# Optimization experiments

Hardware: AMD Instinct MI355X
Metric: run time of the kernel (lower is better)

Reference implementation:

```python
import jax, jax.numpy as jnp
import numpy as np

IN_C = 128
OUT_C = 128
N = 100000
E = 1600000


def spmm(row, col, w, x, n):
    # out[i] = sum_{e: row[e]==i} w[e] * x[col[e]]  (sparse adjacency matmul)
    return jax.ops.segment_sum(w[:, None] * x[col], row, num_segments=n)


def setup_inputs() -> dict:
    key = jax.random.key(0)
    ks = jax.random.split(key, 10)
    x = jax.random.normal(ks[0], (N, IN_C), dtype=jnp.float32)
    row = jax.random.randint(ks[1], (E,), 0, N, dtype=jnp.int32)
    col = jax.random.randint(ks[2], (E,), 0, N, dtype=jnp.int32)
    edge_weight = jax.random.uniform(ks[3], (E,), dtype=jnp.float32)
    s = 1.0 / np.sqrt(IN_C)
    W0 = jax.random.uniform(ks[4], (IN_C, OUT_C), minval=-s, maxval=s, dtype=jnp.float32)
    b0 = jax.random.uniform(ks[5], (OUT_C,), minval=-s, maxval=s, dtype=jnp.float32)
    W1 = jax.random.uniform(ks[6], (IN_C, OUT_C), minval=-s, maxval=s, dtype=jnp.float32)
    b1 = jax.random.uniform(ks[7], (OUT_C,), minval=-s, maxval=s, dtype=jnp.float32)
    W2 = jax.random.uniform(ks[8], (IN_C, OUT_C), minval=-s, maxval=s, dtype=jnp.float32)
    b2 = jax.random.uniform(ks[9], (OUT_C,), minval=-s, maxval=s, dtype=jnp.float32)
    return {"x": x, "row": row, "col": col, "edge_weight": edge_weight,
            "W0": W0, "b0": b0, "W1": W1, "b1": b1, "W2": W2, "b2": b2}


def reference(x, row, col, edge_weight, W0, b0, W1, b1, W2, b2):
    n = x.shape[0]
    # hop 0: plain linear
    x0 = x @ W0 + b0
    # hop 1: linear then one SpMM propagation
    x1 = spmm(row, col, edge_weight, x @ W1 + b1, n)
    # hop 2: linear then two SpMM propagations
    x2 = spmm(row, col, edge_weight,
              spmm(row, col, edge_weight, x @ W2 + b2, n), n)
    return jnp.concatenate([x0, x1, x2], axis=1)  # [N, 3*OUT_C]
```

## Files before the change

kernel.cpp:

```cpp
#include <hip/hip_runtime.h>

typedef __attribute__((ext_vector_type(8))) short bf16x8;
typedef __attribute__((ext_vector_type(4))) float f32x4;
typedef __attribute__((ext_vector_type(2))) float f32x2;
typedef __attribute__((ext_vector_type(2))) uint u32x2;

static inline size_t align256(size_t x) { return (x + 255) & ~size_t(255); }

__device__ inline ushort f2bf(float f) {
  uint u = __float_as_uint(f);
  return (ushort)((u + 0x7FFFu + ((u >> 16) & 1u)) >> 16);
}
__device__ inline float bf2f(ushort h) { return __uint_as_float(((uint)h) << 16); }


__device__ inline uint fp8x4_enc(float a0, float a1, float a2, float a3) {
#if __has_builtin(__builtin_amdgcn_cvt_pk_fp8_f32)
  int v = 0;
  v = __builtin_amdgcn_cvt_pk_fp8_f32(a0, a1, v, false);
  v = __builtin_amdgcn_cvt_pk_fp8_f32(a2, a3, v, true);
  return (uint)v;
#else
  float a[4] = {a0, a1, a2, a3};
  uint r = 0;
#pragma unroll
  for (int k = 0; k < 4; ++k) {
    uint u = __float_as_uint(a[k]);
    uint s = (u >> 24) & 0x80u;
    uint au = u & 0x7FFFFFFFu;
    uint b;
    if (au < 0x3C800000u) {
      b = s;
    } else {
      uint rr = au + 0x7FFFFu + ((au >> 20) & 1u);
      uint e = (rr >> 23) - 120u;
      uint m = (rr >> 20) & 7u;
      b = s | (e << 3) | m;
    }
    r |= b << (8 * k);
  }
  return r;
#endif
}

__device__ inline f32x4 fp8x4_dec(uint u) {
  f32x4 r;
#if __has_builtin(__builtin_amdgcn_cvt_pk_f32_fp8)
  auto lo = __builtin_amdgcn_cvt_pk_f32_fp8((int)u, false);
  auto hi = __builtin_amdgcn_cvt_pk_f32_fp8((int)u, true);
  r[0] = lo[0]; r[1] = lo[1]; r[2] = hi[0]; r[3] = hi[1];
#else
#pragma unroll
  for (int k = 0; k < 4; ++k) {
    uint b = (u >> (8 * k)) & 0xFFu;
    uint f = ((b & 0x80u) << 24) | (((b & 0x7Fu) + (120u << 3)) << 20);
    r[k] = (b & 0x7Fu) ? __uint_as_float(f) : 0.f;
  }
#endif
  return r;
}

__device__ inline float ew_dec(uint u) { return __uint_as_float((u & 0x7FFFu) << 16); }

#define BW_SHIFT 7
#define NBUCK_MAX 1024
#define NCHUNK 256
#define PREP_BLOCKS 96


__global__ __launch_bounds__(512) void build_a_kernel(
    const int* __restrict__ row, int* __restrict__ bcnt,
    int* __restrict__ chunk_hist, int E, int chunk,
    const float* __restrict__ W0, const float* __restrict__ W1,
    const float* __restrict__ W2, ushort* __restrict__ Wt,
    int* __restrict__ done, int* __restrict__ boff, int* __restrict__ gcur,
    int* __restrict__ offp, int n) {
  __shared__ int h[NBUCK_MAX];
  int bid = blockIdx.x;
  int t = threadIdx.x;
  if (bid < NCHUNK) {
    for (int i = t; i < NBUCK_MAX; i += 512) h[i] = 0;
    __syncthreads();
    int c0 = bid * chunk, c1 = min(c0 + chunk, E);
    for (int i = c0 + t; i < c1; i += 512)
      atomicAdd(&h[row[i] >> BW_SHIFT], 1);
    __syncthreads();
    for (int i = t; i < NBUCK_MAX; i += 512) {
      int c = h[i];
      chunk_hist[bid * NBUCK_MAX + i] = c;
      if (c) atomicAdd(&bcnt[i], c);
    }
  } else {
    int i = (bid - NCHUNK) * 512 + t;
    int mat = i >> 14, r = i & 16383;
    int k = r >> 7, c = r & 127;
    const float* W = (mat == 0) ? W0 : (mat == 1) ? W1 : W2;
    Wt[mat * 16384 + c * 128 + k] = f2bf(W[k * 128 + c]);
  }
  __shared__ int ticket;
  __syncthreads();
  if (t == 0) {
    __threadfence();
    ticket = atomicAdd(done, 1);
  }
  __syncthreads();
  if (ticket == (int)gridDim.x - 1) {
    __threadfence();
    int v0 = bcnt[2 * t], v1 = bcnt[2 * t + 1];
    int pair = v0 + v1;
    h[t] = pair;
    __syncthreads();
    for (int o = 1; o < 512; o <<= 1) {
      int a = (t >= o) ? h[t - o] : 0;
      __syncthreads();
      h[t] += a;
      __syncthreads();
    }
    int excl = h[t] - pair;
    boff[2 * t] = excl;          gcur[2 * t] = excl;
    boff[2 * t + 1] = excl + v0; gcur[2 * t + 1] = excl + v0;
    if (t == 511) boff[NBUCK_MAX] = E;
    if (t == 0) offp[n] = E;
  }
}


__global__ __launch_bounds__(512) void bin_scatter(
    const int* __restrict__ row, const int* __restrict__ col,
    const float* __restrict__ w, int* __restrict__ gcur,
    const int* __restrict__ chunk_hist, int2* __restrict__ es_tmp,
    int E, int chunk) {
  __shared__ int lbase[NBUCK_MAX];
  __shared__ int lh[NBUCK_MAX];
  int bid = blockIdx.x;
  int t = threadIdx.x;
  for (int i = t; i < NBUCK_MAX; i += 512) {
    int c = chunk_hist[bid * NBUCK_MAX + i];
    lbase[i] = c ? atomicAdd(&gcur[i], c) : 0;
    lh[i] = 0;
  }
  __syncthreads();
  int c0 = bid * chunk, c1 = min(c0 + chunk, E);
  for (int i = c0 + t; i < c1; i += 512) {
    int r = row[i];
    int b = r >> BW_SHIFT;
    int pos = lbase[b] + atomicAdd(&lh[b], 1);
    es_tmp[pos] = make_int2(((r & 127) << 17) | col[i], __float_as_int(w[i]));
  }
}


__global__ __launch_bounds__(256) void sort_gemm_kernel(
    const int2* __restrict__ es_tmp, const int* __restrict__ boff,
    uint* __restrict__ es, int* __restrict__ offp, int ng,
    const float* __restrict__ x, const ushort* __restrict__ Wt,
    const float* __restrict__ b0, const float* __restrict__ b1,
    const float* __restrict__ b2,
    float* __restrict__ out0, unsigned char* __restrict__ y12, int n) {
  int t = threadIdx.x;
  if ((int)blockIdx.x >= ng) {
    __shared__ int lh[128];
    __shared__ int lex[128];
    int b = (int)blockIdx.x - ng;
    int base = boff[b], cnt = boff[b + 1] - base;
    if (t < 128) lh[t] = 0;
    __syncthreads();
    for (int i = t; i < cnt; i += 256)
      atomicAdd(&lh[(es_tmp[base + i].x >> 17) & 127], 1);
    __syncthreads();
    if (t < 128) lex[t] = lh[t];
    __syncthreads();
    for (int o = 1; o < 128; o <<= 1) {
      int a = (t >= o && t < 128) ? lex[t - o] : 0;
      __syncthreads();
      if (t < 128) lex[t] += a;
      __syncthreads();
    }
    if (t < 128) {
      int v = lh[t];
      int excl = lex[t] - v;
      int node = (b << BW_SHIFT) + t;
      if (node < n) offp[node] = base + excl;
      lh[t] = excl;
    }
    __syncthreads();
    for (int i = t; i < cnt; i += 256) {
      int2 ed = es_tmp[base + i];
      int nl = (ed.x >> 17) & 127;
      int pos = base + atomicAdd(&lh[nl], 1);
      uint wb = (uint)f2bf(__int_as_float(ed.y)) & 0x7FFFu;
      es[pos] = ((uint)(ed.x & 0x1FFFF) << 15) | wb;
    }
    return;
  }
  int w = t >> 6;
  int l = t & 63;
  int lr = l & 15;
  int lg = l >> 4;
  int rows0 = (int)blockIdx.x * 256 + w * 64;

  bf16x8 xf[4][4];
#pragma unroll
  for (int rt = 0; rt < 4; ++rt) {
    int row = rows0 + rt * 16 + lr;
    bool ok = row < n;
    const float* base = x + (size_t)row * 128;
#pragma unroll
    for (int kc = 0; kc < 4; ++kc) {
      float4 a = ok ? *(const float4*)(base + kc * 32 + lg * 8) : make_float4(0, 0, 0, 0);
      float4 c = ok ? *(const float4*)(base + kc * 32 + lg * 8 + 4) : make_float4(0, 0, 0, 0);
      bf16x8 f;
      f[0] = (short)f2bf(a.x); f[1] = (short)f2bf(a.y);
      f[2] = (short)f2bf(a.z); f[3] = (short)f2bf(a.w);
      f[4] = (short)f2bf(c.x); f[5] = (short)f2bf(c.y);
      f[6] = (short)f2bf(c.z); f[7] = (short)f2bf(c.w);
      xf[rt][kc] = f;
    }
  }

  for (int mat = 0; mat < 3; ++mat) {
    const ushort* Wm = Wt + mat * 16384;
    const float* bias = (mat == 0) ? b0 : (mat == 1) ? b1 : b2;
#pragma unroll 1
    for (int ct = 0; ct < 8; ++ct) {
      bf16x8 wf[4];
#pragma unroll
      for (int kc = 0; kc < 4; ++kc)
        wf[kc] = *(const bf16x8*)(Wm + (ct * 16 + lr) * 128 + kc * 32 + lg * 8);
      float4 bb = *(const float4*)(bias + ct * 16 + lg * 4);
      f32x4 acc[4];
#pragma unroll
      for (int rt = 0; rt < 4; ++rt) {
        acc[rt][0] = bb.x; acc[rt][1] = bb.y; acc[rt][2] = bb.z; acc[rt][3] = bb.w;
      }
#pragma unroll
      for (int kc = 0; kc < 4; ++kc)
#pragma unroll
        for (int rt = 0; rt < 4; ++rt)
          acc[rt] = __builtin_amdgcn_mfma_f32_16x16x32_bf16(wf[kc], xf[rt][kc], acc[rt], 0, 0, 0);
#pragma unroll
      for (int rt = 0; rt < 4; ++rt) {
        int row = rows0 + rt * 16 + lr;
        if (row >= n) continue;
        int col = ct * 16 + lg * 4;
        if (mat == 0) {
          __builtin_nontemporal_store(acc[rt], (f32x4*)(out0 + (size_t)row * 384 + col));
        } else {
          uint v8 = fp8x4_enc(acc[rt][0], acc[rt][1], acc[rt][2], acc[rt][3]);
          unsigned char* Y = y12 + (size_t)row * 256 + ((mat == 2) ? 128 : 0) + col;
          *(uint*)Y = v8;
        }
      }
    }
  }
}


__global__ __launch_bounds__(256) void spmm_dual_kernel(
    const unsigned char* __restrict__ y12,
    float* __restrict__ o1,
    ushort* __restrict__ z2,
    const int* __restrict__ off, const uint* __restrict__ es, int n) {
  int node = blockIdx.x * 4 + (threadIdx.x >> 6);
  if (node >= n) return;
  int l = threadIdx.x & 63;
  int s = __builtin_amdgcn_readfirstlane(off[node]);
  int e = __builtin_amdgcn_readfirstlane(off[node + 1]);
  float a0 = 0.f, a1 = 0.f, a2 = 0.f, a3 = 0.f;
  int i = s;
  for (; i + 8 <= e; i += 8) {
    uint u[8];
    float w[8];
#pragma unroll
    for (int j = 0; j < 8; ++j) {
      uint ed = es[i + j];
      w[j] = ew_dec(ed);
      u[j] = *(const uint*)(y12 + (size_t)(ed >> 15) * 256 + l * 4);
    }
#pragma unroll
    for (int j = 0; j < 8; ++j) {
      f32x4 p = fp8x4_dec(u[j]);
      a0 += w[j] * p[0]; a1 += w[j] * p[1];
      a2 += w[j] * p[2]; a3 += w[j] * p[3];
    }
  }
  for (; i < e; ++i) {
    uint ed = es[i];
    float w = ew_dec(ed);
    f32x4 p = fp8x4_dec(*(const uint*)(y12 + (size_t)(ed >> 15) * 256 + l * 4));
    a0 += w * p[0]; a1 += w * p[1]; a2 += w * p[2]; a3 += w * p[3];
  }
  if (l < 32) {
    f32x4 v; v[0] = a0; v[1] = a1; v[2] = a2; v[3] = a3;
    __builtin_nontemporal_store(v, (f32x4*)(o1 + (size_t)node * 384 + l * 4));
  } else {
    u32x2 z;
    z.x = (uint)f2bf(a0) | ((uint)f2bf(a1) << 16);
    z.y = (uint)f2bf(a2) | ((uint)f2bf(a3) << 16);
    *(u32x2*)(z2 + (size_t)node * 128 + (l - 32) * 4) = z;
  }
}


__global__ __launch_bounds__(256) void spmm_single_kernel(
    const ushort* __restrict__ z2,
    float* __restrict__ o2,
    const int* __restrict__ off, const uint* __restrict__ es, int n) {
  int node = blockIdx.x * 4 + (threadIdx.x >> 6);
  if (node >= n) return;
  int l = threadIdx.x & 63;
  int s = __builtin_amdgcn_readfirstlane(off[node]);
  int e = __builtin_amdgcn_readfirstlane(off[node + 1]);
  float a0 = 0.f, a1 = 0.f;
  int i = s;
  for (; i + 8 <= e; i += 8) {
    uint u[8];
    float w[8];
#pragma unroll
    for (int j = 0; j < 8; ++j) {
      uint ed = es[i + j];
      w[j] = ew_dec(ed);
      u[j] = *(const uint*)(z2 + (size_t)(ed >> 15) * 128 + l * 2);
    }
#pragma unroll
    for (int j = 0; j < 8; ++j) {
      a0 += w[j] * bf2f((ushort)u[j]); a1 += w[j] * bf2f((ushort)(u[j] >> 16));
    }
  }
  for (; i < e; ++i) {
    uint ed = es[i];
    float w = ew_dec(ed);
    uint u = *(const uint*)(z2 + (size_t)(ed >> 15) * 128 + l * 2);
    a0 += w * bf2f((ushort)u); a1 += w * bf2f((ushort)(u >> 16));
  }
  f32x2 v; v.x = a0; v.y = a1;
  __builtin_nontemporal_store(v, (f32x2*)(o2 + (size_t)node * 384 + l * 2));
}


extern "C" void kernel_launch(void* const* d_in, const int* in_sizes, int n_in,
                              void* d_out, int out_size, void* d_ws, size_t ws_size,
                              hipStream_t stream) {
  const float* x   = (const float*)d_in[0];
  const int*   row = (const int*)d_in[1];
  const int*   col = (const int*)d_in[2];
  const float* ew  = (const float*)d_in[3];
  const float* W0  = (const float*)d_in[4];
  const float* b0  = (const float*)d_in[5];
  const float* W1  = (const float*)d_in[6];
  const float* b1  = (const float*)d_in[7];
  const float* W2  = (const float*)d_in[8];
  const float* b2  = (const float*)d_in[9];
  float* out = (float*)d_out;

  int n = in_sizes[0] / 128;
  int E = in_sizes[1];

  char* p = (char*)d_ws;
  size_t o = 0;
  unsigned char* y12 = (unsigned char*)(p + o); o = align256(o + (size_t)n * 256);
  ushort* z2  = (ushort*)(p + o); o = align256(o + (size_t)n * 128 * 2);
  ushort* Wt  = (ushort*)(p + o); o = align256(o + (size_t)3 * 16384 * 2);
  int* bcnt   = (int*)(p + o);    o = align256(o + (size_t)(NBUCK_MAX + 1) * 4);
  int* done   = bcnt + NBUCK_MAX;
  int* boff   = (int*)(p + o);    o = align256(o + (size_t)(NBUCK_MAX + 1) * 4);
  int* gcur   = (int*)(p + o);    o = align256(o + (size_t)NBUCK_MAX * 4);
  int* offp   = (int*)(p + o);    o = align256(o + ((size_t)n + 1) * 4);
  int* chist  = (int*)(p + o);    o = align256(o + (size_t)NCHUNK * NBUCK_MAX * 4);
  int2* es_t  = (int2*)(p + o);   o = align256(o + (size_t)E * 8);
  uint* es    = (uint*)(p + o);   o = align256(o + (size_t)E * 4);
  (void)ws_size; (void)n_in; (void)out_size;

  int nbuck = (n + 127) >> 7;
  int ng = (n + 255) / 256;
  int chunk = (E + NCHUNK - 1) / NCHUNK;

  hipMemsetAsync(bcnt, 0, (size_t)(NBUCK_MAX + 1) * 4, stream);

  build_a_kernel<<<NCHUNK + PREP_BLOCKS, 512, 0, stream>>>(
      row, bcnt, chist, E, chunk, W0, W1, W2, Wt, done, boff, gcur, offp, n);

  bin_scatter<<<NCHUNK, 512, 0, stream>>>(row, col, ew, gcur, chist, es_t, E, chunk);

  sort_gemm_kernel<<<ng + nbuck, 256, 0, stream>>>(
      es_t, boff, es, offp, ng,
      x, Wt, b0, b1, b2, out, y12, n);

  spmm_dual_kernel<<<(n + 3) / 4, 256, 0, stream>>>(y12, out + 128, z2,
                                                    offp, es, n);
  spmm_single_kernel<<<(n + 3) / 4, 256, 0, stream>>>(z2, out + 256,
                                                      offp, es, n);
}
```

Baseline: 224.6 us.

## Fuse histogram and bin-scatter into one kernel with a grid-wide flag barrier

Merges the bucket histogram kernel and the bin-scatter kernel into a single launch. The last block to finish computes the prefix sum and publishes a release flag that the histogram blocks spin on, and each block keeps its local histogram in shared memory rather than writing and rereading a per-chunk histogram array. This removes one kernel launch and the chunk_hist global traffic. In exchange it relies on all 352 blocks being co-resident to avoid deadlock and adds spin-wait latency.

```diff
diff --git a/kernel.cpp b/kernel.cpp
--- a/kernel.cpp
+++ b/kernel.cpp
@@ -68,28 +68,28 @@
 #define PREP_BLOCKS 96
 
 
-__global__ __launch_bounds__(512) void build_a_kernel(
-    const int* __restrict__ row, int* __restrict__ bcnt,
-    int* __restrict__ chunk_hist, int E, int chunk,
+__global__ __launch_bounds__(512) void build_ab_kernel(
+    const int* __restrict__ row, const int* __restrict__ col,
+    const float* __restrict__ w, int* __restrict__ bcnt, int E, int chunk,
     const float* __restrict__ W0, const float* __restrict__ W1,
     const float* __restrict__ W2, ushort* __restrict__ Wt,
-    int* __restrict__ done, int* __restrict__ boff, int* __restrict__ gcur,
-    int* __restrict__ offp, int n) {
+    int* __restrict__ done, int* __restrict__ flag,
+    int* __restrict__ boff, int* __restrict__ gcur,
+    int* __restrict__ offp, int2* __restrict__ es_tmp, int n) {
   __shared__ int h[NBUCK_MAX];
+  __shared__ int lbase[NBUCK_MAX];
   int bid = blockIdx.x;
   int t = threadIdx.x;
-  if (bid < NCHUNK) {
+  bool is_hist = (bid < NCHUNK);
+  int c0 = bid * chunk, c1 = min(c0 + chunk, E);
+  if (is_hist) {
     for (int i = t; i < NBUCK_MAX; i += 512) h[i] = 0;
     __syncthreads();
-    int c0 = bid * chunk, c1 = min(c0 + chunk, E);
     for (int i = c0 + t; i < c1; i += 512)
       atomicAdd(&h[row[i] >> BW_SHIFT], 1);
     __syncthreads();
-    for (int i = t; i < NBUCK_MAX; i += 512) {
-      int c = h[i];
-      chunk_hist[bid * NBUCK_MAX + i] = c;
-      if (c) atomicAdd(&bcnt[i], c);
-    }
+    for (int i = t; i < NBUCK_MAX; i += 512)
+      if (h[i]) atomicAdd(&bcnt[i], h[i]);
   } else {
     int i = (bid - NCHUNK) * 512 + t;
     int mat = i >> 14, r = i & 16383;
@@ -108,43 +108,41 @@
     __threadfence();
     int v0 = bcnt[2 * t], v1 = bcnt[2 * t + 1];
     int pair = v0 + v1;
-    h[t] = pair;
+    lbase[t] = pair;
     __syncthreads();
     for (int o = 1; o < 512; o <<= 1) {
-      int a = (t >= o) ? h[t - o] : 0;
+      int a = (t >= o) ? lbase[t - o] : 0;
       __syncthreads();
-      h[t] += a;
+      lbase[t] += a;
       __syncthreads();
     }
-    int excl = h[t] - pair;
+    int excl = lbase[t] - pair;
     boff[2 * t] = excl;          gcur[2 * t] = excl;
     boff[2 * t + 1] = excl + v0; gcur[2 * t + 1] = excl + v0;
     if (t == 511) boff[NBUCK_MAX] = E;
-    if (t == 0) offp[n] = E;
-  }
-}
-
-
-__global__ __launch_bounds__(512) void bin_scatter(
-    const int* __restrict__ row, const int* __restrict__ col,
-    const float* __restrict__ w, int* __restrict__ gcur,
-    const int* __restrict__ chunk_hist, int2* __restrict__ es_tmp,
-    int E, int chunk) {
-  __shared__ int lbase[NBUCK_MAX];
-  __shared__ int lh[NBUCK_MAX];
-  int bid = blockIdx.x;
-  int t = threadIdx.x;
+    if (t == 0) {
+      offp[n] = E;
+      __threadfence();
+      __hip_atomic_store(flag, 1, __ATOMIC_RELEASE, __HIP_MEMORY_SCOPE_AGENT);
+    }
+    __syncthreads();
+  }
+  if (!is_hist) return;
+  if (t == 0) {
+    while (__hip_atomic_load(flag, __ATOMIC_ACQUIRE, __HIP_MEMORY_SCOPE_AGENT) == 0)
+      __builtin_amdgcn_s_sleep(8);
+  }
+  __syncthreads();
   for (int i = t; i < NBUCK_MAX; i += 512) {
-    int c = chunk_hist[bid * NBUCK_MAX + i];
+    int c = h[i];
     lbase[i] = c ? atomicAdd(&gcur[i], c) : 0;
-    lh[i] = 0;
+    h[i] = 0;
   }
   __syncthreads();
-  int c0 = bid * chunk, c1 = min(c0 + chunk, E);
   for (int i = c0 + t; i < c1; i += 512) {
     int r = row[i];
     int b = r >> BW_SHIFT;
-    int pos = lbase[b] + atomicAdd(&lh[b], 1);
+    int pos = lbase[b] + atomicAdd(&h[b], 1);
     es_tmp[pos] = make_int2(((r & 127) << 17) | col[i], __float_as_int(w[i]));
   }
 }
@@ -361,12 +359,12 @@
   unsigned char* y12 = (unsigned char*)(p + o); o = align256(o + (size_t)n * 256);
   ushort* z2  = (ushort*)(p + o); o = align256(o + (size_t)n * 128 * 2);
   ushort* Wt  = (ushort*)(p + o); o = align256(o + (size_t)3 * 16384 * 2);
-  int* bcnt   = (int*)(p + o);    o = align256(o + (size_t)(NBUCK_MAX + 1) * 4);
+  int* bcnt   = (int*)(p + o);    o = align256(o + (size_t)(NBUCK_MAX + 2) * 4);
   int* done   = bcnt + NBUCK_MAX;
+  int* flag   = bcnt + NBUCK_MAX + 1;
   int* boff   = (int*)(p + o);    o = align256(o + (size_t)(NBUCK_MAX + 1) * 4);
   int* gcur   = (int*)(p + o);    o = align256(o + (size_t)NBUCK_MAX * 4);
   int* offp   = (int*)(p + o);    o = align256(o + ((size_t)n + 1) * 4);
-  int* chist  = (int*)(p + o);    o = align256(o + (size_t)NCHUNK * NBUCK_MAX * 4);
   int2* es_t  = (int2*)(p + o);   o = align256(o + (size_t)E * 8);
   uint* es    = (uint*)(p + o);   o = align256(o + (size_t)E * 4);
   (void)ws_size; (void)n_in; (void)out_size;
@@ -375,12 +373,11 @@
   int ng = (n + 255) / 256;
   int chunk = (E + NCHUNK - 1) / NCHUNK;
 
-  hipMemsetAsync(bcnt, 0, (size_t)(NBUCK_MAX + 1) * 4, stream);
-
-  build_a_kernel<<<NCHUNK + PREP_BLOCKS, 512, 0, stream>>>(
-      row, bcnt, chist, E, chunk, W0, W1, W2, Wt, done, boff, gcur, offp, n);
-
-  bin_scatter<<<NCHUNK, 512, 0, stream>>>(row, col, ew, gcur, chist, es_t, E, chunk);
+  hipMemsetAsync(bcnt, 0, (size_t)(NBUCK_MAX + 2) * 4, stream);
+
+  build_ab_kernel<<<NCHUNK + PREP_BLOCKS, 512, 0, stream>>>(
+      row, col, ew, bcnt, E, chunk, W0, W1, W2, Wt, done, flag,
+      boff, gcur, offp, es_t, n);
 
   sort_gemm_kernel<<<ng + nbuck, 256, 0, stream>>>(
       es_t, boff, es, offp, ng,
```

Measured after the change: 254.3 us. +13.2%, slower.
